# Kernel tuning notes

Hardware: AMD Instinct MI355X
Metric: run time of the kernel (lower is better)

The kernel has to match this reference:

```python
import jax, jax.numpy as jnp
import numpy as np

B, L, M, D = 8, 2048, 2048, 256


def setup_inputs() -> dict:
    key = jax.random.key(0)
    k1, k2, k3, k4, k5 = jax.random.split(key, 5)
    inp = jax.random.normal(k1, (B, L, D), dtype=jnp.float32)
    mem = jax.random.normal(k2, (B, M, D), dtype=jnp.float32)
    mask = jnp.ones((B, M), dtype=jnp.float32)
    # Learned parameters (Linear(D, 1, bias=False) -> weight vector of shape [D])
    w_input = jax.random.normal(k3, (D,), dtype=jnp.float32) / np.sqrt(D)
    w_memory = jax.random.normal(k4, (D,), dtype=jnp.float32) / np.sqrt(D)
    dot_scale = jax.random.uniform(k5, (D,), dtype=jnp.float32, minval=0.0, maxval=1.0 / np.sqrt(D))
    return {"input": inp, "memory": mem, "mask": mask,
            "w_input": w_input, "w_memory": w_memory, "dot_scale": dot_scale}


def reference(input, memory, mask, w_input, w_memory, dot_scale):
    # dropout with p=0.0 / eval mode -> identity
    input_dot = jnp.einsum('bld,d->bl', input, w_input)[:, :, None]      # [B, L, 1]
    memory_dot = jnp.einsum('bmd,d->bm', memory, w_memory)[:, None, :]   # [B, 1, M]
    cross_dot = jnp.einsum('bld,bmd->blm', input * dot_scale, memory)    # [B, L, M]
    att = input_dot + memory_dot + cross_dot                             # [B, L, M]
    att = att - 1e30 * (1.0 - mask[:, None, :])
    weight_one = jax.nn.softmax(att, axis=-1)                            # [B, L, M]
    output_one = jnp.einsum('blm,bmd->bld', weight_one, memory)          # [B, L, D]
    weight_two = jax.nn.softmax(jnp.max(att, axis=-1), axis=-1)[:, None, :]  # [B, 1, L]
    output_two = jnp.einsum('bol,bld->bod', weight_two, input)           # [B, 1, D]
    return jnp.concatenate(
        [input, output_one, input * output_one, output_two * output_one], axis=-1)
```

## Files before the change

kernel.cpp:

```cpp
#include <hip/hip_runtime.h>
#include <hip/hip_bf16.h>


typedef __bf16 bf16_t;
typedef bf16_t bf16x4 __attribute__((ext_vector_type(4)));
typedef bf16_t bf16x8 __attribute__((ext_vector_type(8)));
typedef float  f32x16 __attribute__((ext_vector_type(16)));
typedef unsigned int u32x2 __attribute__((ext_vector_type(2)));
typedef unsigned int u32x4 __attribute__((ext_vector_type(4)));

#define NB 8
#define NL 2048
#define NM 2048
#define ND 256
#define OUTW 1024
#define MT 64
#define MH 1024
#define NIT 16
#define LT 128
#define MEMT_X0 8388608u
#define FLASH_LDS 133120

__device__ __forceinline__ unsigned omap(unsigned x) {
    return ((x >> 10) << 12) | (x & 1023u);
}

__device__ __forceinline__ void dma16(const void* g, void* l) {
    __builtin_amdgcn_global_load_lds(
        (const __attribute__((address_space(1))) unsigned int*)g,
        (__attribute__((address_space(3))) unsigned int*)l, 16, 0, 0);
}

__global__ __launch_bounds__(256) void prep_kernel(
    const float* __restrict__ memory, const float* __restrict__ mask,
    const float* __restrict__ w_memory,
    float* __restrict__ ws_mbias, float* __restrict__ ws_numden,
    char* __restrict__ outc)
{
    __shared__ __align__(16) bf16_t lds[32 * 264];

    int b  = blockIdx.x >> 6;
    int mc = blockIdx.x & 63;
    int t  = threadIdx.x, w = t >> 6, lane = t & 63;

    if (blockIdx.x == 0) {
        for (int k = t; k < 2056; k += 256) ws_numden[k] = 0.f;
    }

    float4 wv = *(const float4*)(w_memory + lane * 4);

    #pragma unroll
    for (int it = 0; it < 8; ++it) {
        int rloc = it * 4 + w;
        int row  = b * NM + mc * 32 + rloc;
        float4 v = *(const float4*)(memory + (size_t)row * ND + lane * 4);
        float s = v.x * wv.x + v.y * wv.y + v.z * wv.z + v.w * wv.w;
        #pragma unroll
        for (int off = 1; off < 64; off <<= 1) s += __shfl_xor(s, off, 64);
        if (lane == 0) ws_mbias[row] = s - 1e30f * (1.0f - mask[row]);
        bf16x4 bv;
        bv[0] = (bf16_t)v.x; bv[1] = (bf16_t)v.y;
        bv[2] = (bf16_t)v.z; bv[3] = (bf16_t)v.w;
        *(bf16x4*)(&lds[rloc * 264 + lane * 4]) = bv;
    }
    __syncthreads();

    {
        unsigned xbase = ((unsigned)(b * 64 + mc)) * 16384u;
        int c = t & 31, h5 = (t >> 5) & 1, ksh = t >> 6;
        #pragma unroll
        for (int r = 0; r < 4; ++r) {
            bf16x8 g = *(const bf16x8*)(&lds[c * 264 + (4 * r + ksh) * 16 + h5 * 8]);
            *(bf16x8*)(outc + omap(xbase + r * 4096u + (unsigned)t * 16u)) = g;
        }
    }

    int d = t;
    #pragma unroll
    for (int mc4 = 0; mc4 < 4; ++mc4) {
        bf16x8 pk;
        #pragma unroll
        for (int j = 0; j < 8; ++j) pk[j] = lds[(mc4 * 8 + j) * 264 + d];
        unsigned x = MEMT_X0 +
            2u * ((((unsigned)(b * 256 + mc * 4 + mc4)) * ND + d) * 8);
        *(bf16x8*)(outc + omap(x)) = pk;
    }
}

__global__ __launch_bounds__(512, 2) void flash_kernel(
    const float* __restrict__ input, const float* __restrict__ dot_scale,
    const float* __restrict__ w_input, const float* __restrict__ ws_mbias,
    const char* __restrict__ outc, float* __restrict__ out,
    float* __restrict__ ws_l, float* __restrict__ ws_m,
    float* __restrict__ ws_idot)
{
    extern __shared__ __align__(16) char smem[];

    int bid = blockIdx.x;
    int half = bid & 1, b = (bid >> 1) & 7, lt = bid >> 4;
    int l0 = lt * LT;
    int m_base = half * MH;
    int t = threadIdx.x, w = t >> 6, lane = t & 63;
    int gw = w & 3, grp = w >> 2;
    int c = lane & 31, h = lane >> 5;

    const float* qrow = input + (size_t)(b * NL + l0 + gw * 32 + c) * ND;
    bool do_idot = (half == 0) && (grp == 0);
    float idot_s = 0.f;
    bf16x8 qf[16];
    #pragma unroll
    for (int ks = 0; ks < 16; ++ks) {
        int d0 = ks * 16 + h * 8;
        float4 a0 = *(const float4*)(qrow + d0);
        float4 a1 = *(const float4*)(qrow + d0 + 4);
        float4 s0 = *(const float4*)(dot_scale + d0);
        float4 s1 = *(const float4*)(dot_scale + d0 + 4);
        if (do_idot) {
            float4 w0 = *(const float4*)(w_input + d0);
            float4 w1 = *(const float4*)(w_input + d0 + 4);
            idot_s += a0.x * w0.x + a0.y * w0.y + a0.z * w0.z + a0.w * w0.w
                    + a1.x * w1.x + a1.y * w1.y + a1.z * w1.z + a1.w * w1.w;
        }
        qf[ks][0] = (bf16_t)(a0.x * s0.x); qf[ks][1] = (bf16_t)(a0.y * s0.y);
        qf[ks][2] = (bf16_t)(a0.z * s0.z); qf[ks][3] = (bf16_t)(a0.w * s0.w);
        qf[ks][4] = (bf16_t)(a1.x * s1.x); qf[ks][5] = (bf16_t)(a1.y * s1.y);
        qf[ks][6] = (bf16_t)(a1.z * s1.z); qf[ks][7] = (bf16_t)(a1.w * s1.w);
    }
    if (do_idot) {
        idot_s += __shfl_xor(idot_s, 32, 64);
        if (lane < 32) ws_idot[b * NL + l0 + gw * 32 + lane] = idot_s;
    }

    unsigned xk = ((unsigned)(b * 64 + half * 32 + grp)) * 16384u + (unsigned)lane * 16u;
    const char* kg = outc + omap(xk);
    unsigned xv = MEMT_X0 +
        2u * ((((unsigned)(b * 256 + (m_base >> 3) + grp * 4 + h)) * ND + c) * 8);
    const char* vg = outc + omap(xv);

    char* buf0 = smem;
    char* buf1 = smem + 65536;

    #define STAGE(nbuf) do {                                                  \
        _Pragma("unroll")                                                     \
        for (int j = 0; j < 4; ++j) {                                         \
            int i = gw * 4 + j;                                               \
            int ks = i >> 3, dt = i & 7;                                      \
            dma16(kg + i * 4096, (nbuf) + grp * 16384 + i * 1024);            \
            dma16(vg + ks * 32768 + (dt >> 1) * 4096 + (dt & 1) * 512,        \
                  (nbuf) + 32768 + grp * 16384 + i * 1024);                   \
        }                                                                     \
        kg += 131072; vg += 131072; } while (0)

    STAGE(buf0);

    f32x16 oaccT[8];
    #pragma unroll
    for (int i = 0; i < 8; ++i)
        #pragma unroll
        for (int r = 0; r < 16; ++r) oaccT[i][r] = 0.f;
    float lsum = 0.f, mmax = -3e38f;

    const float* mb_base = ws_mbias + b * NM;

    #pragma unroll 1
    for (int it = 0; it < NIT; ++it) {
        int m0 = m_base + it * MT + grp * 32;
        asm volatile("s_waitcnt vmcnt(0)" ::: "memory");
        __syncthreads();
        const char* cb = (it & 1) ? buf1 : buf0;
        char* nb = (it & 1) ? buf0 : buf1;
        const bf16_t* kb = (const bf16_t*)(cb + grp * 16384);
        const bf16_t* vb = (const bf16_t*)(cb + 32768 + grp * 16384);
        if (it + 1 < NIT) {
            STAGE(nb);
        }
        const float* mrow = mb_base + m0 + 4 * h;
        float4 mbv0 = *(const float4*)(mrow);
        float4 mbv1 = *(const float4*)(mrow + 8);
        float4 mbv2 = *(const float4*)(mrow + 16);
        float4 mbv3 = *(const float4*)(mrow + 24);
        f32x16 S;
        #pragma unroll
        for (int r = 0; r < 16; ++r) S[r] = 0.f;
        #pragma unroll
        for (int ks = 0; ks < 16; ++ks) {
            bf16x8 k0 = *(const bf16x8*)(kb + ks * 512 + lane * 8);
            S = __builtin_amdgcn_mfma_f32_32x32x16_bf16(k0, qf[ks], S, 0, 0, 0);
        }
        u32x2 own[4];
        #pragma unroll
        for (int g = 0; g < 4; ++g) {
            float4 mbv = (g == 0) ? mbv0 : (g == 1) ? mbv1 : (g == 2) ? mbv2 : mbv3;
            bf16x4 tq;
            #pragma unroll
            for (int q = 0; q < 4; ++q) {
                float v = S[g * 4 + q] +
                          ((q == 0) ? mbv.x : (q == 1) ? mbv.y : (q == 2) ? mbv.z : mbv.w);
                mmax = fmaxf(mmax, v);
                float e = __expf(v);
                lsum += e;
                tq[q] = (bf16_t)e;
            }
            own[g] = __builtin_bit_cast(u32x2, tq);
        }
        #pragma unroll
        for (int ks = 0; ks < 2; ++ks) {
            unsigned oAlo = own[2 * ks].x,     oAhi = own[2 * ks].y;
            unsigned oBlo = own[2 * ks + 1].x, oBhi = own[2 * ks + 1].y;
            unsigned slo = h ? oAlo : oBlo;
            unsigned shi = h ? oAhi : oBhi;
            unsigned rlo = (unsigned)__shfl_xor((int)slo, 32, 64);
            unsigned rhi = (unsigned)__shfl_xor((int)shi, 32, 64);
            unsigned mlo = h ? oBlo : oAlo;
            unsigned mhi = h ? oBhi : oAhi;
            u32x4 uu;
            uu.x = h ? rlo : mlo;
            uu.y = h ? rhi : mhi;
            uu.z = h ? mlo : rlo;
            uu.w = h ? mhi : rhi;
            bf16x8 pb = __builtin_bit_cast(bf16x8, uu);
            #pragma unroll
            for (int dt = 0; dt < 8; ++dt) {
                bf16x8 vv = *(const bf16x8*)(vb + (ks * 8 + dt) * 512 + lane * 8);
                oaccT[dt] = __builtin_amdgcn_mfma_f32_32x32x16_bf16(vv, pb, oaccT[dt], 0, 0, 0);
            }
        }
    }
    #undef STAGE

    __syncthreads();
    if (grp == 1) {
        float* dst = (float*)(smem + gw * 32768);
        #pragma unroll
        for (int dt = 0; dt < 8; ++dt) {
            #pragma unroll
            for (int q = 0; q < 4; ++q) {
                float4 v4;
                v4.x = oaccT[dt][q * 4 + 0]; v4.y = oaccT[dt][q * 4 + 1];
                v4.z = oaccT[dt][q * 4 + 2]; v4.w = oaccT[dt][q * 4 + 3];
                *(float4*)(dst + dt * 1024 + q * 256 + lane * 4) = v4;
            }
        }
        float* aux = (float*)(smem + 131072 + gw * 512);
        aux[lane] = lsum;
        aux[64 + lane] = mmax;
    }
    __syncthreads();
    if (grp == 0) {
        const float* src = (const float*)(smem + gw * 32768);
        #pragma unroll
        for (int dt = 0; dt < 8; ++dt) {
            #pragma unroll
            for (int q = 0; q < 4; ++q) {
                float4 v4 = *(const float4*)(src + dt * 1024 + q * 256 + lane * 4);
                oaccT[dt][q * 4 + 0] += v4.x; oaccT[dt][q * 4 + 1] += v4.y;
                oaccT[dt][q * 4 + 2] += v4.z; oaccT[dt][q * 4 + 3] += v4.w;
            }
        }
        const float* aux = (const float*)(smem + 131072 + gw * 512);
        lsum += aux[lane];
        mmax = fmaxf(mmax, aux[64 + lane]);
    }
    __syncthreads();
    if (grp == 0) {
        mmax = fmaxf(mmax, __shfl_xor(mmax, 32, 64));
        lsum += __shfl_xor(lsum, 32, 64);
        if (lane < 32) {
            int row = b * NL + l0 + gw * 32 + lane;
            ws_l[half * (NB * NL) + row] = lsum;
            ws_m[half * (NB * NL) + row] = mmax;
        }
        float* patch = (float*)(smem + gw * 4352);
        float* oseg = out + (size_t)(b * NL + l0 + gw * 32) * OUTW + ND * (1 + half);
        #pragma unroll
        for (int dt = 0; dt < 8; ++dt) {
            asm volatile("s_waitcnt lgkmcnt(0)" ::: "memory");
            #pragma unroll
            for (int r = 0; r < 16; ++r)
                patch[((r & 3) + 8 * (r >> 2) + 4 * h) * 33 + c] = oaccT[dt][r];
            asm volatile("s_waitcnt lgkmcnt(0)" ::: "memory");
            #pragma unroll
            for (int rr = 0; rr < 16; ++rr) {
                float val = patch[c * 33 + rr * 2 + h];
                oseg[(size_t)(rr * 2 + h) * OUTW + dt * 32 + c] = val;
            }
        }
    }
}

__global__ __launch_bounds__(256) void o2_kernel(
    const float* __restrict__ input, const float* __restrict__ ws_idot,
    const float* __restrict__ ws_m, float* __restrict__ ws_num,
    float* __restrict__ ws_den)
{
    __shared__ float4 red[256];
    int b = blockIdx.x >> 5, slice = blockIdx.x & 31;
    int t = threadIdx.x;
    int lgrp = t >> 6, d4 = (t & 63) * 4;
    float4 acc = {0.f, 0.f, 0.f, 0.f};
    float esum = 0.f;
    for (int i = 0; i < 16; ++i) {
        int row = b * NL + slice * 64 + lgrp * 16 + i;
        float e = __expf(ws_idot[row] + fmaxf(ws_m[row], ws_m[NB * NL + row]));
        float4 v = *(const float4*)(input + (size_t)row * ND + d4);
        acc.x += e * v.x; acc.y += e * v.y;
        acc.z += e * v.z; acc.w += e * v.w;
        esum += e;
    }
    red[t] = acc;
    __syncthreads();
    if (t < 64) {
        float4 a0 = red[t], a1 = red[t + 64], a2 = red[t + 128], a3 = red[t + 192];
        float* dst = ws_num + b * ND + t * 4;
        atomicAdd(dst + 0, a0.x + a1.x + a2.x + a3.x);
        atomicAdd(dst + 1, a0.y + a1.y + a2.y + a3.y);
        atomicAdd(dst + 2, a0.z + a1.z + a2.z + a3.z);
        atomicAdd(dst + 3, a0.w + a1.w + a2.w + a3.w);
    }
    if ((t & 63) == 0) atomicAdd(ws_den + b, esum);
}

__global__ __launch_bounds__(256) void assembly_kernel(
    const float* __restrict__ input, const float* __restrict__ ws_num,
    const float* __restrict__ ws_den, const float* __restrict__ ws_l,
    float* __restrict__ out)
{
    size_t tid = (size_t)blockIdx.x * 256 + threadIdx.x;
    size_t row = tid >> 6;
    int d = (int)(tid & 63) * 4;
    int b = (int)(row >> 11);
    float inv  = 1.0f / (ws_l[row] + ws_l[NB * NL + row]);
    float dinv = 1.0f / ws_den[b];
    float* po = out + row * OUTW;
    float4 in = *(const float4*)(input + row * ND + d);
    float4 pa = *(const float4*)(po + ND + d);
    float4 pb = *(const float4*)(po + 2 * ND + d);
    float4 nu = *(const float4*)(ws_num + b * ND + d);
    float4 o1;
    o1.x = (pa.x + pb.x) * inv; o1.y = (pa.y + pb.y) * inv;
    o1.z = (pa.z + pb.z) * inv; o1.w = (pa.w + pb.w) * inv;
    float4 o2v;
    o2v.x = nu.x * dinv; o2v.y = nu.y * dinv;
    o2v.z = nu.z * dinv; o2v.w = nu.w * dinv;
    *(float4*)(po + d) = in;
    *(float4*)(po + ND + d) = o1;
    float4 q;
    q.x = in.x * o1.x; q.y = in.y * o1.y; q.z = in.z * o1.z; q.w = in.w * o1.w;
    *(float4*)(po + 2 * ND + d) = q;
    float4 r;
    r.x = o2v.x * o1.x; r.y = o2v.y * o1.y; r.z = o2v.z * o1.z; r.w = o2v.w * o1.w;
    *(float4*)(po + 3 * ND + d) = r;
}

extern "C" void kernel_launch(void* const* d_in, const int* in_sizes, int n_in,
                              void* d_out, int out_size, void* d_ws, size_t ws_size,
                              hipStream_t stream) {
    const float* input     = (const float*)d_in[0];
    const float* memory    = (const float*)d_in[1];
    const float* mask      = (const float*)d_in[2];
    const float* w_input   = (const float*)d_in[3];
    const float* w_memory  = (const float*)d_in[4];
    const float* dot_scale = (const float*)d_in[5];
    float* out = (float*)d_out;
    char* outc = (char*)d_out;
    float* ws  = (float*)d_ws;

    float* ws_idot  = ws;
    float* ws_mbias = ws + 16384;
    float* ws_l     = ws + 32768;
    float* ws_m     = ws + 65536;
    float* ws_num   = ws + 98304;
    float* ws_den   = ws + 100352;

    prep_kernel<<<512, 256, 0, stream>>>(memory, mask, w_memory, ws_mbias,
                                         ws_num, outc);
    flash_kernel<<<256, 512, FLASH_LDS, stream>>>(input, dot_scale, w_input,
                                                  ws_mbias, outc, out,
                                                  ws_l, ws_m, ws_idot);
    o2_kernel<<<256, 256, 0, stream>>>(input, ws_idot, ws_m, ws_num, ws_den);
    assembly_kernel<<<4096, 256, 0, stream>>>(input, ws_num, ws_den, ws_l, out);
}
```

Measured before the change: 190.9 us.

## Split K/V staging and triple-buffer K to prefetch two tiles ahead

Separates the K and V tile DMA into distinct staging macros, triple-buffers K (prefetched two iterations ahead) while V stays double-buffered, and relaxes the per-iteration wait from vmcnt(0) to vmcnt(4). The goal is to hide global-to-LDS load latency behind the MFMA work instead of draining all outstanding loads every iteration. LDS use grows from about 130KB to 160KB, and the counted-wait logic depends on exact issue ordering, so it is fragile.

```diff
diff --git a/kernel.cpp b/kernel.cpp
--- a/kernel.cpp
+++ b/kernel.cpp
@@ -19,7 +19,7 @@
 #define NIT 16
 #define LT 128
 #define MEMT_X0 8388608u
-#define FLASH_LDS 133120
+#define FLASH_LDS 163840
 
 __device__ __forceinline__ unsigned omap(unsigned x) {
     return ((x >> 10) << 12) | (x & 1023u);
@@ -137,21 +137,33 @@
         2u * ((((unsigned)(b * 256 + (m_base >> 3) + grp * 4 + h)) * ND + c) * 8);
     const char* vg = outc + omap(xv);
 
-    char* buf0 = smem;
-    char* buf1 = smem + 65536;
-
-    #define STAGE(nbuf) do {                                                  \
+    char* kbase = smem;
+    char* vbase = smem + 98304;
+
+    #define STAGE_K(nbuf) do {                                                \
+        _Pragma("unroll")                                                     \
+        for (int j = 0; j < 4; ++j) {                                         \
+            int i = gw * 4 + j;                                               \
+            dma16(kg + i * 4096, (nbuf) + grp * 16384 + i * 1024);            \
+        }                                                                     \
+        kg += 131072; } while (0)
+
+    #define STAGE_V(nbuf) do {                                                \
         _Pragma("unroll")                                                     \
         for (int j = 0; j < 4; ++j) {                                         \
             int i = gw * 4 + j;                                               \
             int ks = i >> 3, dt = i & 7;                                      \
-            dma16(kg + i * 4096, (nbuf) + grp * 16384 + i * 1024);            \
             dma16(vg + ks * 32768 + (dt >> 1) * 4096 + (dt & 1) * 512,        \
-                  (nbuf) + 32768 + grp * 16384 + i * 1024);                   \
+                  (nbuf) + grp * 16384 + i * 1024);                           \
         }                                                                     \
-        kg += 131072; vg += 131072; } while (0)
-
-    STAGE(buf0);
+        vg += 131072; } while (0)
+
+    STAGE_K(kbase);
+    asm volatile("" ::: "memory");
+    STAGE_V(vbase);
+    asm volatile("" ::: "memory");
+    STAGE_K(kbase + 32768);
+    asm volatile("" ::: "memory");
 
     f32x16 oaccT[8];
     #pragma unroll
@@ -162,23 +174,27 @@
 
     const float* mb_base = ws_mbias + b * NM;
 
+    unsigned kcur = 0, kst = 65536;
+    unsigned vcur = 0, vst = 32768;
+
     #pragma unroll 1
     for (int it = 0; it < NIT; ++it) {
         int m0 = m_base + it * MT + grp * 32;
-        asm volatile("s_waitcnt vmcnt(0)" ::: "memory");
+        asm volatile("s_waitcnt vmcnt(4)" ::: "memory");
+        if (it == NIT - 1) asm volatile("s_waitcnt vmcnt(0)" ::: "memory");
         __syncthreads();
-        const char* cb = (it & 1) ? buf1 : buf0;
-        char* nb = (it & 1) ? buf0 : buf1;
-        const bf16_t* kb = (const bf16_t*)(cb + grp * 16384);
-        const bf16_t* vb = (const bf16_t*)(cb + 32768 + grp * 16384);
-        if (it + 1 < NIT) {
-            STAGE(nb);
-        }
+        const bf16_t* kb = (const bf16_t*)(kbase + kcur + grp * 16384);
+        const bf16_t* vb = (const bf16_t*)(vbase + vcur + grp * 16384);
         const float* mrow = mb_base + m0 + 4 * h;
         float4 mbv0 = *(const float4*)(mrow);
         float4 mbv1 = *(const float4*)(mrow + 8);
         float4 mbv2 = *(const float4*)(mrow + 16);
         float4 mbv3 = *(const float4*)(mrow + 24);
+        asm volatile("" ::: "memory");
+        if (it + 1 < NIT) { STAGE_V(vbase + vst); }
+        asm volatile("" ::: "memory");
+        if (it + 2 < NIT) { STAGE_K(kbase + kst); }
+        asm volatile("" ::: "memory");
         f32x16 S;
         #pragma unroll
         for (int r = 0; r < 16; ++r) S[r] = 0.f;
@@ -225,8 +241,12 @@
                 oaccT[dt] = __builtin_amdgcn_mfma_f32_32x32x16_bf16(vv, pb, oaccT[dt], 0, 0, 0);
             }
         }
-    }
-    #undef STAGE
+        kcur = (kcur == 65536u) ? 0u : kcur + 32768u;
+        kst  = (kst  == 65536u) ? 0u : kst + 32768u;
+        vcur ^= 32768u; vst ^= 32768u;
+    }
+    #undef STAGE_K
+    #undef STAGE_V
 
     __syncthreads();
     if (grp == 1) {
```

Result: slower. 196.6 us (+3.0%).

## Split flash attention over four M-quarters per block with atomic merging

Applied to the files above, without the earlier changes.

The flash kernel now launches 512 blocks of 256 threads, each handling one quarter of the memory dimension with a 32-wide tile. Partial softmax sums, maxima and output accumulators are merged with global atomics (float add, and max via an order-preserving uint key) instead of the in-block LDS reduction between two warp groups. Prep now zeroes the accumulator workspace and the output slices. This raises block count and cuts LDS per block to improve occupancy, at the cost of many float atomics on output rows. The result also becomes non-deterministic.

```diff
diff --git a/kernel.cpp b/kernel.cpp
--- a/kernel.cpp
+++ b/kernel.cpp
@@ -14,12 +14,11 @@
 #define NM 2048
 #define ND 256
 #define OUTW 1024
-#define MT 64
-#define MH 1024
+#define MT 32
 #define NIT 16
 #define LT 128
 #define MEMT_X0 8388608u
-#define FLASH_LDS 133120
+#define FLASH_LDS 65536
 
 __device__ __forceinline__ unsigned omap(unsigned x) {
     return ((x >> 10) << 12) | (x & 1023u);
@@ -34,8 +33,8 @@
 __global__ __launch_bounds__(256) void prep_kernel(
     const float* __restrict__ memory, const float* __restrict__ mask,
     const float* __restrict__ w_memory,
-    float* __restrict__ ws_mbias, float* __restrict__ ws_numden,
-    char* __restrict__ outc)
+    float* __restrict__ ws_mbias, float* __restrict__ ws_lm,
+    float* __restrict__ ws_numden, char* __restrict__ outc)
 {
     __shared__ __align__(16) bf16_t lds[32 * 264];
 
@@ -45,6 +44,18 @@
 
     if (blockIdx.x == 0) {
         for (int k = t; k < 2056; k += 256) ws_numden[k] = 0.f;
+    }
+    if (t < 128) ws_lm[blockIdx.x * 128 + t] = 0.f;
+    {
+        float* outf = (float*)outc;
+        float4 z = {0.f, 0.f, 0.f, 0.f};
+        int row0 = blockIdx.x * 32;
+        #pragma unroll
+        for (int k = 0; k < 16; ++k) {
+            int idx = k * 256 + t;
+            int r = idx >> 7, e = idx & 127;
+            *(float4*)(outf + (size_t)(row0 + r) * OUTW + 256 + e * 4) = z;
+        }
     }
 
     float4 wv = *(const float4*)(w_memory + lane * 4);
@@ -87,7 +98,7 @@
     }
 }
 
-__global__ __launch_bounds__(512, 2) void flash_kernel(
+__global__ __launch_bounds__(256, 2) void flash_kernel(
     const float* __restrict__ input, const float* __restrict__ dot_scale,
     const float* __restrict__ w_input, const float* __restrict__ ws_mbias,
     const char* __restrict__ outc, float* __restrict__ out,
@@ -97,15 +108,15 @@
     extern __shared__ __align__(16) char smem[];
 
     int bid = blockIdx.x;
-    int half = bid & 1, b = (bid >> 1) & 7, lt = bid >> 4;
+    int lt = bid >> 5, b = (bid >> 2) & 7, q = bid & 3;
     int l0 = lt * LT;
-    int m_base = half * MH;
+    int slot = q >> 1;
     int t = threadIdx.x, w = t >> 6, lane = t & 63;
-    int gw = w & 3, grp = w >> 2;
+    int gw = w;
     int c = lane & 31, h = lane >> 5;
 
     const float* qrow = input + (size_t)(b * NL + l0 + gw * 32 + c) * ND;
-    bool do_idot = (half == 0) && (grp == 0);
+    bool do_idot = (q == 0);
     float idot_s = 0.f;
     bf16x8 qf[16];
     #pragma unroll
@@ -131,25 +142,25 @@
         if (lane < 32) ws_idot[b * NL + l0 + gw * 32 + lane] = idot_s;
     }
 
-    unsigned xk = ((unsigned)(b * 64 + half * 32 + grp)) * 16384u + (unsigned)lane * 16u;
+    unsigned xk = ((unsigned)(b * 64 + q * 16)) * 16384u + (unsigned)lane * 16u;
     const char* kg = outc + omap(xk);
     unsigned xv = MEMT_X0 +
-        2u * ((((unsigned)(b * 256 + (m_base >> 3) + grp * 4 + h)) * ND + c) * 8);
+        2u * ((((unsigned)(b * 256 + q * 64 + h)) * ND + c) * 8);
     const char* vg = outc + omap(xv);
 
     char* buf0 = smem;
-    char* buf1 = smem + 65536;
+    char* buf1 = smem + 32768;
 
     #define STAGE(nbuf) do {                                                  \
         _Pragma("unroll")                                                     \
         for (int j = 0; j < 4; ++j) {                                         \
             int i = gw * 4 + j;                                               \
             int ks = i >> 3, dt = i & 7;                                      \
-            dma16(kg + i * 4096, (nbuf) + grp * 16384 + i * 1024);            \
+            dma16(kg + i * 4096, (nbuf) + i * 1024);                          \
             dma16(vg + ks * 32768 + (dt >> 1) * 4096 + (dt & 1) * 512,        \
-                  (nbuf) + 32768 + grp * 16384 + i * 1024);                   \
+                  (nbuf) + 16384 + i * 1024);                                 \
         }                                                                     \
-        kg += 131072; vg += 131072; } while (0)
+        kg += 65536; vg += 65536; } while (0)
 
     STAGE(buf0);
 
@@ -164,16 +175,14 @@
 
     #pragma unroll 1
     for (int it = 0; it < NIT; ++it) {
-        int m0 = m_base + it * MT + grp * 32;
+        int m0 = q * 512 + it * MT;
         asm volatile("s_waitcnt vmcnt(0)" ::: "memory");
         __syncthreads();
         const char* cb = (it & 1) ? buf1 : buf0;
         char* nb = (it & 1) ? buf0 : buf1;
-        const bf16_t* kb = (const bf16_t*)(cb + grp * 16384);
-        const bf16_t* vb = (const bf16_t*)(cb + 32768 + grp * 16384);
-        if (it + 1 < NIT) {
-            STAGE(nb);
-        }
+        const bf16_t* kb = (const bf16_t*)cb;
+        const bf16_t* vb = (const bf16_t*)(cb + 16384);
+        if (it + 1 < NIT) { STAGE(nb); }
         const float* mrow = mb_base + m0 + 4 * h;
         float4 mbv0 = *(const float4*)(mrow);
         float4 mbv1 = *(const float4*)(mrow + 8);
@@ -193,13 +202,13 @@
             float4 mbv = (g == 0) ? mbv0 : (g == 1) ? mbv1 : (g == 2) ? mbv2 : mbv3;
             bf16x4 tq;
             #pragma unroll
-            for (int q = 0; q < 4; ++q) {
-                float v = S[g * 4 + q] +
-                          ((q == 0) ? mbv.x : (q == 1) ? mbv.y : (q == 2) ? mbv.z : mbv.w);
+            for (int qq = 0; qq < 4; ++qq) {
+                float v = S[g * 4 + qq] +
+                          ((qq == 0) ? mbv.x : (qq == 1) ? mbv.y : (qq == 2) ? mbv.z : mbv.w);
                 mmax = fmaxf(mmax, v);
                 float e = __expf(v);
                 lsum += e;
-                tq[q] = (bf16_t)e;
+                tq[qq] = (bf16_t)e;
             }
             own[g] = __builtin_bit_cast(u32x2, tq);
         }
@@ -229,49 +238,19 @@
     #undef STAGE
 
     __syncthreads();
-    if (grp == 1) {
-        float* dst = (float*)(smem + gw * 32768);
-        #pragma unroll
-        for (int dt = 0; dt < 8; ++dt) {
-            #pragma unroll
-            for (int q = 0; q < 4; ++q) {
-                float4 v4;
-                v4.x = oaccT[dt][q * 4 + 0]; v4.y = oaccT[dt][q * 4 + 1];
-                v4.z = oaccT[dt][q * 4 + 2]; v4.w = oaccT[dt][q * 4 + 3];
-                *(float4*)(dst + dt * 1024 + q * 256 + lane * 4) = v4;
-            }
-        }
-        float* aux = (float*)(smem + 131072 + gw * 512);
-        aux[lane] = lsum;
-        aux[64 + lane] = mmax;
-    }
-    __syncthreads();
-    if (grp == 0) {
-        const float* src = (const float*)(smem + gw * 32768);
-        #pragma unroll
-        for (int dt = 0; dt < 8; ++dt) {
-            #pragma unroll
-            for (int q = 0; q < 4; ++q) {
-                float4 v4 = *(const float4*)(src + dt * 1024 + q * 256 + lane * 4);
-                oaccT[dt][q * 4 + 0] += v4.x; oaccT[dt][q * 4 + 1] += v4.y;
-                oaccT[dt][q * 4 + 2] += v4.z; oaccT[dt][q * 4 + 3] += v4.w;
-            }
-        }
-        const float* aux = (const float*)(smem + 131072 + gw * 512);
-        lsum += aux[lane];
-        mmax = fmaxf(mmax, aux[64 + lane]);
-    }
-    __syncthreads();
-    if (grp == 0) {
-        mmax = fmaxf(mmax, __shfl_xor(mmax, 32, 64));
-        lsum += __shfl_xor(lsum, 32, 64);
-        if (lane < 32) {
-            int row = b * NL + l0 + gw * 32 + lane;
-            ws_l[half * (NB * NL) + row] = lsum;
-            ws_m[half * (NB * NL) + row] = mmax;
-        }
+
+    mmax = fmaxf(mmax, __shfl_xor(mmax, 32, 64));
+    lsum += __shfl_xor(lsum, 32, 64);
+    if (lane < 32) {
+        int row = b * NL + l0 + gw * 32 + lane;
+        atomicAdd(&ws_l[slot * (NB * NL) + row], lsum);
+        unsigned u = __float_as_uint(mmax);
+        unsigned key = (u >> 31) ? ~u : (u | 0x80000000u);
+        atomicMax((unsigned*)ws_m + slot * (NB * NL) + row, key);
+    }
+    {
         float* patch = (float*)(smem + gw * 4352);
-        float* oseg = out + (size_t)(b * NL + l0 + gw * 32) * OUTW + ND * (1 + half);
+        float* oseg = out + (size_t)(b * NL + l0 + gw * 32) * OUTW + ND * (1 + slot);
         #pragma unroll
         for (int dt = 0; dt < 8; ++dt) {
             asm volatile("s_waitcnt lgkmcnt(0)" ::: "memory");
@@ -282,7 +261,7 @@
             #pragma unroll
             for (int rr = 0; rr < 16; ++rr) {
                 float val = patch[c * 33 + rr * 2 + h];
-                oseg[(size_t)(rr * 2 + h) * OUTW + dt * 32 + c] = val;
+                atomicAdd(&oseg[(size_t)(rr * 2 + h) * OUTW + dt * 32 + c], val);
             }
         }
     }
@@ -294,6 +273,7 @@
     float* __restrict__ ws_den)
 {
     __shared__ float4 red[256];
+    const unsigned* wm = (const unsigned*)ws_m;
     int b = blockIdx.x >> 5, slice = blockIdx.x & 31;
     int t = threadIdx.x;
     int lgrp = t >> 6, d4 = (t & 63) * 4;
@@ -301,7 +281,10 @@
     float esum = 0.f;
     for (int i = 0; i < 16; ++i) {
         int row = b * NL + slice * 64 + lgrp * 16 + i;
-        float e = __expf(ws_idot[row] + fmaxf(ws_m[row], ws_m[NB * NL + row]));
+        unsigned k0 = wm[row], k1 = wm[NB * NL + row];
+        unsigned kk = k0 > k1 ? k0 : k1;
+        float m = __uint_as_float((kk >> 31) ? (kk & 0x7FFFFFFFu) : ~kk);
+        float e = __expf(ws_idot[row] + m);
         float4 v = *(const float4*)(input + (size_t)row * ND + d4);
         acc.x += e * v.x; acc.y += e * v.y;
         acc.z += e * v.z; acc.w += e * v.w;
@@ -344,9 +327,9 @@
     o2v.z = nu.z * dinv; o2v.w = nu.w * dinv;
     *(float4*)(po + d) = in;
     *(float4*)(po + ND + d) = o1;
-    float4 q;
-    q.x = in.x * o1.x; q.y = in.y * o1.y; q.z = in.z * o1.z; q.w = in.w * o1.w;
-    *(float4*)(po + 2 * ND + d) = q;
+    float4 qv;
+    qv.x = in.x * o1.x; qv.y = in.y * o1.y; qv.z = in.z * o1.z; qv.w = in.w * o1.w;
+    *(float4*)(po + 2 * ND + d) = qv;
     float4 r;
     r.x = o2v.x * o1.x; r.y = o2v.y * o1.y; r.z = o2v.z * o1.z; r.w = o2v.w * o1.w;
     *(float4*)(po + 3 * ND + d) = r;
@@ -373,8 +356,9 @@
     float* ws_den   = ws + 100352;
 
     prep_kernel<<<512, 256, 0, stream>>>(memory, mask, w_memory, ws_mbias,
+                                         ws_l ,
                                          ws_num, outc);
-    flash_kernel<<<256, 512, FLASH_LDS, stream>>>(input, dot_scale, w_input,
+    flash_kernel<<<512, 256, FLASH_LDS, stream>>>(input, dot_scale, w_input,
                                                   ws_mbias, outc, out,
                                                   ws_l, ws_m, ws_idot);
     o2_kernel<<<256, 256, 0, stream>>>(input, ws_idot, ws_m, ws_num, ws_den);
```

New measurement: 225.9 us. 18.4% more time.
